# Kernel optimization log

Hardware: AMD Instinct MI355X
Metric: run time of the kernel (lower is better)

The kernel has to match this reference:

```python
import jax, jax.numpy as jnp
import numpy as np

SQRT_2PI = 2.5066282  # sqrt(2*3.1415926), matching the TF constant

def _gaussian(x, mean, std):
    return 1.0 / std / SQRT_2PI * jnp.exp(-0.5 * (x - mean) ** 2 / std ** 2)

def setup_inputs() -> dict:
    key = jax.random.key(0)
    ks = jax.random.split(key, 7)
    B, L, D, H, K = 4, 2048, 256, 8, 64
    return {
        "x": jax.random.normal(ks[0], (B, L, D), dtype=jnp.float32),
        "Wq": jax.random.normal(ks[1], (D, H * K), dtype=jnp.float32) * (2.0 / (D + H * K)) ** 0.5,
        "bq": jnp.zeros((H,), dtype=jnp.float32),
        "Wk": jax.random.normal(ks[2], (D, H * K), dtype=jnp.float32) * (2.0 / (D + H * K)) ** 0.5,
        "bk": jnp.zeros((H,), dtype=jnp.float32),
        "prior_mean": jax.random.uniform(ks[3], (H,), dtype=jnp.float32, minval=-2048.0, maxval=2048.0),
        "log_prior_std": jnp.full((H,), np.log(2048.0 / 4.0), dtype=jnp.float32),
    }

def reference(x, Wq, bq, Wk, bk, prior_mean, log_prior_std):
    B, L, D = x.shape
    H = bq.shape[0]
    Kd = Wq.shape[1] // H
    # projections; per-head scalar bias (tf.repeat(bias, head_dim))
    q = (x @ Wq).reshape(B, L, H, Kd) + bq[None, None, :, None]
    k = (x @ Wk).reshape(B, L, H, Kd) + bk[None, None, :, None]
    # relative-position distance matrix [L, L] (slice of the max_length matrix)
    pos = jnp.arange(L, dtype=jnp.float32)
    dist = pos[None, :] - pos[:, None]
    # per-head Gaussian prior [H, L, L]
    std = jnp.exp(log_prior_std)
    prior = _gaussian(dist[None, :, :], prior_mean[:, None, None], std[:, None, None])
    # scaled QK^T, modulated by prior, softmax over keys
    scores = jnp.einsum('bqhk,bmhk->bhqm', q, k) * (float(Kd) ** -0.5)
    attn = jax.nn.softmax(scores * prior[None], axis=-1)  # [B, H, L, L]
    # distance expectation instead of attn @ V
    out = jnp.sum(attn * dist[None, None, :, :], axis=-1)  # [B, H, L]
    return out.transpose(0, 2, 1)  # [B, L, H]
```

## Files before the change

### kernel.cpp

```cpp
#include <hip/hip_runtime.h>
#include <hip/hip_bf16.h>

#define LB 2048
#define DB 256
#define HB 8
#define BH 32
#define NG 19
#define NROW 48
#define NCK 16

typedef __attribute__((ext_vector_type(8))) short short8;
typedef __attribute__((ext_vector_type(4))) short short4v;
typedef __attribute__((ext_vector_type(4))) float floatx4;

static __device__ __forceinline__ short bfbits(float f) {
    __hip_bfloat16 h = __float2bfloat16(f);
    return *reinterpret_cast<short*>(&h);
}

__global__ __launch_bounds__(256) void prep_misc(
    const float* __restrict__ Wq, const float* __restrict__ Wk,
    const float* __restrict__ pm, const float* __restrict__ ls,
    __hip_bfloat16* __restrict__ wb, __hip_bfloat16* __restrict__ prtF)
{
    if (blockIdx.x < 64) {
        const int blk = blockIdx.x;
        const float* W = (blk & 32) ? Wk : Wq;
        const int nbase = (blk & 31) * 16;
#pragma unroll
        for (int cc = 0; cc < 2; ++cc) {
            const int c  = threadIdx.x + cc * 256;
            const int n  = nbase + (c & 15);
            const int k0 = (c >> 4) * 8;
            short8 o;
#pragma unroll
            for (int e = 0; e < 8; ++e) o[e] = bfbits(W[(size_t)(k0 + e) * 512 + n]);
            *(reinterpret_cast<short8*>(wb + (size_t)blk * 4096) + c) = o;
        }
        return;
    }
    const int blk2 = blockIdx.x - 64;
    const int h    = blk2 / 12;
    const int rem  = blk2 - h * 12;
    const int gt   = rem >> 2;
    const int msq  = rem & 3;
    const int wv   = threadIdx.x >> 6;
    const int l    = threadIdx.x & 63;

    const float mu        = pm[h];
    const float inv_sigma = __expf(-ls[h]);
    const float coef = 0.125f * inv_sigma * (1.0f / 2.5066282f);

    const int row = gt * 16 + (l & 15);
#pragma unroll
    for (int it = 0; it < 4; ++it) {
        const int ms = msq * 16 + wv * 4 + it;
        const int m0 = ms * 32 + (l >> 4) * 8;
        short8 o;
#pragma unroll
        for (int e = 0; e < 8; ++e) {
            float val = 0.f;
            if (row < 38) {
                const int g = (row < 19) ? row : row - 19;
                const float d = (float)(m0 + e - 128 * g + 128);
                const float t = (d - mu) * inv_sigma;
                const float P = coef * __expf(-0.5f * t * t);
                val = (row < 19) ? P : P * d;
            }
            o[e] = bfbits(val);
        }
        reinterpret_cast<short8*>(prtF)[(size_t)((h * 3 + gt) * 64 + ms) * 64 + l] = o;
    }
}

__global__ __launch_bounds__(256) void proj_fused(
    const float* __restrict__ x, const __hip_bfloat16* __restrict__ wb,
    const float* __restrict__ bq, const float* __restrict__ bk,
    __hip_bfloat16* __restrict__ qf, __hip_bfloat16* __restrict__ kT)
{
    __shared__ __align__(16) char smem[64 * 264 * 2];
    auto xs = reinterpret_cast<__hip_bfloat16(*)[264]>(smem);
    auto ot = reinterpret_cast<__hip_bfloat16(*)[136]>(smem);

    const int rt   = blockIdx.x;
    const int cg   = blockIdx.y;
    const int wave = threadIdx.x >> 6;
    const int lane = threadIdx.x & 63;
    const int kg   = lane >> 4;
    const int l15  = lane & 15;

#pragma unroll
    for (int it = 0; it < 16; ++it) {
        const int idx = threadIdx.x + it * 256;
        const int row = idx >> 6;
        const int k4  = (idx & 63) * 4;
        const float4 v = *reinterpret_cast<const float4*>(x + ((size_t)(rt * 64 + row)) * DB + k4);
        short4v o;
        o[0] = bfbits(v.x); o[1] = bfbits(v.y); o[2] = bfbits(v.z); o[3] = bfbits(v.w);
        *reinterpret_cast<short4v*>(&xs[row][k4]) = o;
    }
    __syncthreads();

    short8 a[8];
    {
        const __hip_bfloat16* xr = &xs[wave * 16 + l15][0];
#pragma unroll
        for (int kb = 0; kb < 8; ++kb)
            a[kb] = *reinterpret_cast<const short8*>(xr + kb * 32 + (lane >> 4) * 8);
    }
    __syncthreads();

    const int b_   = rt >> 5;
    const int gct0 = cg * 8;
    const short8* wp = reinterpret_cast<const short8*>(wb) + lane;

    short8 wA[8], wB[8];
#pragma unroll
    for (int kb = 0; kb < 8; ++kb) wA[kb] = wp[(size_t)(gct0 * 8 + kb) * 64];

#define PROJ_STEP(CURW, NXTW, CT)                                                     \
    {                                                                                 \
        if ((CT) < 7) {                                                               \
            _Pragma("unroll")                                                         \
            for (int kb = 0; kb < 8; ++kb)                                            \
                NXTW[kb] = wp[(size_t)((gct0 + (CT) + 1) * 8 + kb) * 64];             \
        }                                                                             \
        floatx4 acc = {0.f, 0.f, 0.f, 0.f};                                           \
        _Pragma("unroll")                                                             \
        for (int kb = 0; kb < 8; ++kb)                                                \
            acc = __builtin_amdgcn_mfma_f32_16x16x32_bf16(CURW[kb], a[kb], acc, 0, 0, 0); \
        const int h   = ((gct0 + (CT)) & 31) >> 2;                                    \
        const float bias = (cg < 4 ? bq : bk)[h];                                     \
        short4v o;                                                                    \
        _Pragma("unroll")                                                             \
        for (int r = 0; r < 4; ++r) o[r] = bfbits(acc[r] + bias);                     \
        *reinterpret_cast<short4v*>(&ot[wave * 16 + l15][(CT) * 16 + 4 * kg]) = o;    \
    }

    PROJ_STEP(wA, wB, 0)
    PROJ_STEP(wB, wA, 1)
    PROJ_STEP(wA, wB, 2)
    PROJ_STEP(wB, wA, 3)
    PROJ_STEP(wA, wB, 4)
    PROJ_STEP(wB, wA, 5)
    PROJ_STEP(wA, wB, 6)
    PROJ_STEP(wB, wA, 7)
#undef PROJ_STEP

    __syncthreads();

    if (cg < 4) {
        const int h0 = (cg & 3) * 2;
        const int rbase = (rt & 31) * 64;
#pragma unroll
        for (int it = 0; it < 8; ++it) {
            const int cidx = threadIdx.x + it * 256;
            const int row  = cidx >> 5;
            const int sub  = cidx & 31;
            const int hoff = sub >> 4;
            const int ch64 = (sub & 15) * 4;
            const short4v v = *reinterpret_cast<const short4v*>(&ot[row][sub * 4]);
            const size_t dst = (((size_t)(b_ * HB + h0 + hoff) << 11) + rbase + row) * 64 + ch64;
            *reinterpret_cast<short4v*>(qf + dst) = v;
        }
    } else {
        const int hoff = wave >> 1;
        const int msb  = wave & 1;
        const int h0   = (cg & 3) * 2;
        const int bh   = b_ * HB + h0 + hoff;
        const int msG  = (rt & 31) * 2 + msb;
        const int rowb = msb * 32 + (lane >> 4) * 8;
        const int colb = hoff * 64 + l15;
#pragma unroll
        for (int ct = 0; ct < 4; ++ct) {
            short8 o;
#pragma unroll
            for (int e = 0; e < 8; ++e)
                o[e] = *reinterpret_cast<const short*>(&ot[rowb + e][colb + ct * 16]);
            reinterpret_cast<short8*>(kT)[(size_t)((bh * 4 + ct) * 64 + msG) * 64 + lane] = o;
        }
    }
}

__global__ __launch_bounds__(256, 2) void conv_mfma(
    const __hip_bfloat16* __restrict__ prtF, const __hip_bfloat16* __restrict__ kT,
    float* __restrict__ gpart)
{
    const int bh   = blockIdx.x;
    const int wv   = threadIdx.x >> 6;
    const int lane = threadIdx.x & 63;
    const int ck   = blockIdx.y * 4 + wv;
    const int h    = bh & 7;

    const short8* A = reinterpret_cast<const short8*>(prtF);
    const short8* B = reinterpret_cast<const short8*>(kT);

    floatx4 acc[3][4];
#pragma unroll
    for (int gt = 0; gt < 3; ++gt)
#pragma unroll
        for (int ct = 0; ct < 4; ++ct) acc[gt][ct] = (floatx4){0.f, 0.f, 0.f, 0.f};

#pragma unroll
    for (int s = 0; s < 4; ++s) {
        const int ms = ck * 4 + s;
        short8 af[3], bf[4];
#pragma unroll
        for (int gt = 0; gt < 3; ++gt)
            af[gt] = A[(size_t)((h * 3 + gt) * 64 + ms) * 64 + lane];
#pragma unroll
        for (int ct = 0; ct < 4; ++ct)
            bf[ct] = B[(size_t)((bh * 4 + ct) * 64 + ms) * 64 + lane];
#pragma unroll
        for (int gt = 0; gt < 3; ++gt)
#pragma unroll
            for (int ct = 0; ct < 4; ++ct)
                acc[gt][ct] = __builtin_amdgcn_mfma_f32_16x16x32_bf16(af[gt], bf[ct], acc[gt][ct], 0, 0, 0);
    }

    const int kg = lane >> 4, l15 = lane & 15;
    float* gp = gpart + (size_t)(bh * NCK + ck) * (NROW * 64);
#pragma unroll
    for (int gt = 0; gt < 3; ++gt)
#pragma unroll
        for (int ct = 0; ct < 4; ++ct)
#pragma unroll
            for (int r = 0; r < 4; ++r)
                gp[(gt * 16 + 4 * kg + r) * 64 + ct * 16 + l15] = acc[gt][ct][r];
}

__global__ __launch_bounds__(256) void conv_combine(const float* __restrict__ gpart,
                                                    float* __restrict__ gw)
{
    const int j   = blockIdx.x * 256 + threadIdx.x;
    const int bh  = j / 3072;
    const int idx = j - bh * 3072;
    const float* gp = gpart + (size_t)bh * NCK * 3072 + idx;
    float s = 0.f;
#pragma unroll
    for (int c = 0; c < NCK; ++c) s += gp[(size_t)c * 3072];
    gw[j] = s;
}

__global__ __launch_bounds__(256) void final_kernel(
    const __hip_bfloat16* __restrict__ qf, const float* __restrict__ gw,
    float* __restrict__ out)
{
    const int row = blockIdx.x * 16 + (threadIdx.x >> 4);
    const int l15 = threadIdx.x & 15;
    const int bh  = row >> 11;
    const int i   = row & (LB - 1);
    const int b   = bh >> 3;
    const int h   = bh & 7;

    const short4v q4 = reinterpret_cast<const short4v*>(qf)[(size_t)row * 16 + l15];
    float q[4];
#pragma unroll
    for (int e = 0; e < 4; ++e) {
        const unsigned short u16 = (unsigned short)q4[e];
        const unsigned int bits = ((unsigned int)u16) << 16;
        q[e] = __builtin_bit_cast(float, bits);
    }

    const int   cell = i >> 7;
    const float u  = (float)(i & 127) * (1.0f / 128.0f);
    const float u2 = u * u, u3 = u2 * u;
    const float c0 = -0.5f * u + u2 - 0.5f * u3;
    const float c1 = 1.0f - 2.5f * u2 + 1.5f * u3;
    const float c2 = 0.5f * u + 2.0f * u2 - 1.5f * u3;
    const float c3 = -0.5f * u2 + 0.5f * u3;

    const float4* g4 = reinterpret_cast<const float4*>(gw + (size_t)bh * 3072) + l15;
    const float4 n0 = g4[(cell + 0) * 16], n1 = g4[(cell + 1) * 16];
    const float4 n2 = g4[(cell + 2) * 16], n3 = g4[(cell + 3) * 16];
    const float4 w0 = g4[(19 + cell + 0) * 16], w1 = g4[(19 + cell + 1) * 16];
    const float4 w2 = g4[(19 + cell + 2) * 16], w3 = g4[(19 + cell + 3) * 16];

    float D = q[0] * (c0 * n0.x + c1 * n1.x + c2 * n2.x + c3 * n3.x)
            + q[1] * (c0 * n0.y + c1 * n1.y + c2 * n2.y + c3 * n3.y)
            + q[2] * (c0 * n0.z + c1 * n1.z + c2 * n2.z + c3 * n3.z)
            + q[3] * (c0 * n0.w + c1 * n1.w + c2 * n2.w + c3 * n3.w);
    float N = q[0] * (c0 * w0.x + c1 * w1.x + c2 * w2.x + c3 * w3.x)
            + q[1] * (c0 * w0.y + c1 * w1.y + c2 * w2.y + c3 * w3.y)
            + q[2] * (c0 * w0.z + c1 * w1.z + c2 * w2.z + c3 * w3.z)
            + q[3] * (c0 * w0.w + c1 * w1.w + c2 * w2.w + c3 * w3.w);

#pragma unroll
    for (int off = 8; off >= 1; off >>= 1) {
        D += __shfl_xor(D, off, 64);
        N += __shfl_xor(N, off, 64);
    }
    if (l15 == 0) {
        const float C = (float)(2096128 - 2048 * i);
        out[((size_t)(b * LB + i)) * HB + h] = (C + N) / (2048.0f + D);
    }
}

extern "C" void kernel_launch(void* const* d_in, const int* in_sizes, int n_in,
                              void* d_out, int out_size, void* d_ws, size_t ws_size,
                              hipStream_t stream) {
    const float* x  = (const float*)d_in[0];
    const float* Wq = (const float*)d_in[1];
    const float* bq = (const float*)d_in[2];
    const float* Wk = (const float*)d_in[3];
    const float* bk = (const float*)d_in[4];
    const float* pm = (const float*)d_in[5];
    const float* ls = (const float*)d_in[6];
    float* out = (float*)d_out;

    char* w = (char*)d_ws;
    __hip_bfloat16* wbuf = (__hip_bfloat16*)w;  w += (size_t)64 * 4096 * 2;
    __hip_bfloat16* prtF = (__hip_bfloat16*)w;  w += (size_t)24 * 64 * 64 * 8 * 2;
    __hip_bfloat16* qf   = (__hip_bfloat16*)w;  w += (size_t)BH * LB * 64 * 2;
    __hip_bfloat16* kT   = (__hip_bfloat16*)w;  w += (size_t)BH * 4 * 64 * 64 * 8 * 2;
    float*          gpart = (float*)w;          w += (size_t)BH * NCK * NROW * 64 * 4;
    float*          gw    = (float*)w;

    prep_misc<<<dim3(160), dim3(256), 0, stream>>>(Wq, Wk, pm, ls, wbuf, prtF);
    proj_fused<<<dim3(128, 8), dim3(256), 0, stream>>>(x, wbuf, bq, bk, qf, kT);
    conv_mfma<<<dim3(32, 4), dim3(256), 0, stream>>>(prtF, kT, gpart);
    conv_combine<<<dim3(384), dim3(256), 0, stream>>>(gpart, gw);
    final_kernel<<<dim3(4096), dim3(256), 0, stream>>>(qf, gw, out);
}
```

Baseline: 43.58 us.

## Fuse Q/K projection per row tile and fold conv reduction into LDS

The projection kernel now computes all Q and K columns for a 32-row tile in one 512-thread block, so x is read and converted once instead of eight times across column groups. The conv kernel is launched with one block per batch-head, and each wave loops over four chunks. Partial sums are reduced through shared memory, which removes the separate combine kernel and its global partial buffer. The cost is that the conv stage now runs only 32 blocks, cutting parallelism on a many-CU GPU, and the projection block uses a larger LDS footprint.

```diff
diff --git a/kernel.cpp b/kernel.cpp
--- a/kernel.cpp
+++ b/kernel.cpp
@@ -73,28 +73,32 @@
     }
 }
 
-__global__ __launch_bounds__(256) void proj_fused(
+__global__ __launch_bounds__(512, 4) void proj_all(
     const float* __restrict__ x, const __hip_bfloat16* __restrict__ wb,
     const float* __restrict__ bq, const float* __restrict__ bk,
     __hip_bfloat16* __restrict__ qf, __hip_bfloat16* __restrict__ kT)
 {
-    __shared__ __align__(16) char smem[64 * 264 * 2];
+    __shared__ __align__(16) char smem[32 * 1032 * 2];
     auto xs = reinterpret_cast<__hip_bfloat16(*)[264]>(smem);
-    auto ot = reinterpret_cast<__hip_bfloat16(*)[136]>(smem);
-
-    const int rt   = blockIdx.x;
-    const int cg   = blockIdx.y;
-    const int wave = threadIdx.x >> 6;
-    const int lane = threadIdx.x & 63;
+    auto ot = reinterpret_cast<__hip_bfloat16(*)[1032]>(smem);
+
+    const int nrt  = blockIdx.x;
+    const int tid  = threadIdx.x;
+    const int w    = tid >> 6;
+    const int lane = tid & 63;
     const int kg   = lane >> 4;
     const int l15  = lane & 15;
-
-#pragma unroll
-    for (int it = 0; it < 16; ++it) {
-        const int idx = threadIdx.x + it * 256;
+    const int rg   = w & 1;
+    const int qu   = w >> 1;
+    const int b_   = nrt >> 6;
+    const int msG  = nrt & 63;
+
+#pragma unroll
+    for (int it = 0; it < 4; ++it) {
+        const int idx = tid + it * 512;
         const int row = idx >> 6;
         const int k4  = (idx & 63) * 4;
-        const float4 v = *reinterpret_cast<const float4*>(x + ((size_t)(rt * 64 + row)) * DB + k4);
+        const float4 v = *reinterpret_cast<const float4*>(x + ((size_t)(nrt * 32 + row)) * DB + k4);
         short4v o;
         o[0] = bfbits(v.x); o[1] = bfbits(v.y); o[2] = bfbits(v.z); o[3] = bfbits(v.w);
         *reinterpret_cast<short4v*>(&xs[row][k4]) = o;
@@ -103,15 +107,14 @@
 
     short8 a[8];
     {
-        const __hip_bfloat16* xr = &xs[wave * 16 + l15][0];
+        const __hip_bfloat16* xr = &xs[rg * 16 + l15][0];
 #pragma unroll
         for (int kb = 0; kb < 8; ++kb)
-            a[kb] = *reinterpret_cast<const short8*>(xr + kb * 32 + (lane >> 4) * 8);
+            a[kb] = *reinterpret_cast<const short8*>(xr + kb * 32 + kg * 8);
     }
     __syncthreads();
 
-    const int b_   = rt >> 5;
-    const int gct0 = cg * 8;
+    const int gct0 = qu * 16;
     const short8* wp = reinterpret_cast<const short8*>(wb) + lane;
 
     short8 wA[8], wB[8];
@@ -120,7 +123,7 @@
 
 #define PROJ_STEP(CURW, NXTW, CT)                                                     \
     {                                                                                 \
-        if ((CT) < 7) {                                                               \
+        if ((CT) < 15) {                                                              \
             _Pragma("unroll")                                                         \
             for (int kb = 0; kb < 8; ++kb)                                            \
                 NXTW[kb] = wp[(size_t)((gct0 + (CT) + 1) * 8 + kb) * 64];             \
@@ -129,12 +132,13 @@
         _Pragma("unroll")                                                             \
         for (int kb = 0; kb < 8; ++kb)                                                \
             acc = __builtin_amdgcn_mfma_f32_16x16x32_bf16(CURW[kb], a[kb], acc, 0, 0, 0); \
-        const int h   = ((gct0 + (CT)) & 31) >> 2;                                    \
-        const float bias = (cg < 4 ? bq : bk)[h];                                     \
+        const int gct = gct0 + (CT);                                                  \
+        const int h   = (gct & 31) >> 2;                                              \
+        const float bias = (gct < 32 ? bq : bk)[h];                                   \
         short4v o;                                                                    \
         _Pragma("unroll")                                                             \
         for (int r = 0; r < 4; ++r) o[r] = bfbits(acc[r] + bias);                     \
-        *reinterpret_cast<short4v*>(&ot[wave * 16 + l15][(CT) * 16 + 4 * kg]) = o;    \
+        *reinterpret_cast<short4v*>(&ot[rg * 16 + l15][gct * 16 + 4 * kg]) = o;       \
     }
 
     PROJ_STEP(wA, wB, 0)
@@ -145,52 +149,60 @@
     PROJ_STEP(wB, wA, 5)
     PROJ_STEP(wA, wB, 6)
     PROJ_STEP(wB, wA, 7)
+    PROJ_STEP(wA, wB, 8)
+    PROJ_STEP(wB, wA, 9)
+    PROJ_STEP(wA, wB, 10)
+    PROJ_STEP(wB, wA, 11)
+    PROJ_STEP(wA, wB, 12)
+    PROJ_STEP(wB, wA, 13)
+    PROJ_STEP(wA, wB, 14)
+    PROJ_STEP(wB, wA, 15)
 #undef PROJ_STEP
 
     __syncthreads();
 
-    if (cg < 4) {
-        const int h0 = (cg & 3) * 2;
-        const int rbase = (rt & 31) * 64;
-#pragma unroll
-        for (int it = 0; it < 8; ++it) {
-            const int cidx = threadIdx.x + it * 256;
-            const int row  = cidx >> 5;
-            const int sub  = cidx & 31;
-            const int hoff = sub >> 4;
-            const int ch64 = (sub & 15) * 4;
-            const short4v v = *reinterpret_cast<const short4v*>(&ot[row][sub * 4]);
-            const size_t dst = (((size_t)(b_ * HB + h0 + hoff) << 11) + rbase + row) * 64 + ch64;
-            *reinterpret_cast<short4v*>(qf + dst) = v;
-        }
-    } else {
-        const int hoff = wave >> 1;
-        const int msb  = wave & 1;
-        const int h0   = (cg & 3) * 2;
-        const int bh   = b_ * HB + h0 + hoff;
-        const int msG  = (rt & 31) * 2 + msb;
-        const int rowb = msb * 32 + (lane >> 4) * 8;
-        const int colb = hoff * 64 + l15;
-#pragma unroll
-        for (int ct = 0; ct < 4; ++ct) {
+#pragma unroll
+    for (int it = 0; it < 8; ++it) {
+        const int cidx = tid + it * 512;
+        const int row  = cidx >> 7;
+        const int sub  = cidx & 127;
+        const int h    = sub >> 4;
+        const int ch64 = (sub & 15) * 4;
+        const short4v v = *reinterpret_cast<const short4v*>(&ot[row][sub * 4]);
+        const size_t dst = (((size_t)(b_ * HB + h) << 11) + msG * 32 + row) * 64 + ch64;
+        *reinterpret_cast<short4v*>(qf + dst) = v;
+    }
+
+    {
+        const int f  = w * 4;
+#pragma unroll
+        for (int ff = 0; ff < 4; ++ff) {
+            const int h  = (f + ff) >> 2;
+            const int ct = (f + ff) & 3;
+            const int bh = b_ * HB + h;
+            const int colb = 512 + h * 64 + ct * 16 + l15;
+            const int rowb = kg * 8;
             short8 o;
 #pragma unroll
             for (int e = 0; e < 8; ++e)
-                o[e] = *reinterpret_cast<const short*>(&ot[rowb + e][colb + ct * 16]);
+                o[e] = *reinterpret_cast<const short*>(&ot[rowb + e][colb]);
             reinterpret_cast<short8*>(kT)[(size_t)((bh * 4 + ct) * 64 + msG) * 64 + lane] = o;
         }
     }
 }
 
-__global__ __launch_bounds__(256, 2) void conv_mfma(
+__global__ __launch_bounds__(256) void conv_fused(
     const __hip_bfloat16* __restrict__ prtF, const __hip_bfloat16* __restrict__ kT,
-    float* __restrict__ gpart)
+    float* __restrict__ gw)
 {
+    __shared__ float red[4][3072];
+
     const int bh   = blockIdx.x;
     const int wv   = threadIdx.x >> 6;
     const int lane = threadIdx.x & 63;
-    const int ck   = blockIdx.y * 4 + wv;
     const int h    = bh & 7;
+    const int kg   = lane >> 4;
+    const int l15  = lane & 15;
 
     const short8* A = reinterpret_cast<const short8*>(prtF);
     const short8* B = reinterpret_cast<const short8*>(kT);
@@ -202,44 +214,37 @@
         for (int ct = 0; ct < 4; ++ct) acc[gt][ct] = (floatx4){0.f, 0.f, 0.f, 0.f};
 
 #pragma unroll
-    for (int s = 0; s < 4; ++s) {
-        const int ms = ck * 4 + s;
-        short8 af[3], bf[4];
-#pragma unroll
-        for (int gt = 0; gt < 3; ++gt)
-            af[gt] = A[(size_t)((h * 3 + gt) * 64 + ms) * 64 + lane];
+    for (int cki = 0; cki < 4; ++cki) {
+        const int ck = wv * 4 + cki;
+#pragma unroll
+        for (int s = 0; s < 4; ++s) {
+            const int ms = ck * 4 + s;
+            short8 af[3], bf[4];
+#pragma unroll
+            for (int gt = 0; gt < 3; ++gt)
+                af[gt] = A[(size_t)((h * 3 + gt) * 64 + ms) * 64 + lane];
+#pragma unroll
+            for (int ct = 0; ct < 4; ++ct)
+                bf[ct] = B[(size_t)((bh * 4 + ct) * 64 + ms) * 64 + lane];
+#pragma unroll
+            for (int gt = 0; gt < 3; ++gt)
+#pragma unroll
+                for (int ct = 0; ct < 4; ++ct)
+                    acc[gt][ct] = __builtin_amdgcn_mfma_f32_16x16x32_bf16(af[gt], bf[ct], acc[gt][ct], 0, 0, 0);
+        }
+    }
+
+#pragma unroll
+    for (int gt = 0; gt < 3; ++gt)
 #pragma unroll
         for (int ct = 0; ct < 4; ++ct)
-            bf[ct] = B[(size_t)((bh * 4 + ct) * 64 + ms) * 64 + lane];
-#pragma unroll
-        for (int gt = 0; gt < 3; ++gt)
-#pragma unroll
-            for (int ct = 0; ct < 4; ++ct)
-                acc[gt][ct] = __builtin_amdgcn_mfma_f32_16x16x32_bf16(af[gt], bf[ct], acc[gt][ct], 0, 0, 0);
-    }
-
-    const int kg = lane >> 4, l15 = lane & 15;
-    float* gp = gpart + (size_t)(bh * NCK + ck) * (NROW * 64);
-#pragma unroll
-    for (int gt = 0; gt < 3; ++gt)
-#pragma unroll
-        for (int ct = 0; ct < 4; ++ct)
 #pragma unroll
             for (int r = 0; r < 4; ++r)
-                gp[(gt * 16 + 4 * kg + r) * 64 + ct * 16 + l15] = acc[gt][ct][r];
-}
-
-__global__ __launch_bounds__(256) void conv_combine(const float* __restrict__ gpart,
-                                                    float* __restrict__ gw)
-{
-    const int j   = blockIdx.x * 256 + threadIdx.x;
-    const int bh  = j / 3072;
-    const int idx = j - bh * 3072;
-    const float* gp = gpart + (size_t)bh * NCK * 3072 + idx;
-    float s = 0.f;
-#pragma unroll
-    for (int c = 0; c < NCK; ++c) s += gp[(size_t)c * 3072];
-    gw[j] = s;
+                red[wv][(gt * 16 + 4 * kg + r) * 64 + ct * 16 + l15] = acc[gt][ct][r];
+    __syncthreads();
+
+    for (int j = threadIdx.x; j < 3072; j += 256)
+        gw[(size_t)bh * 3072 + j] = red[0][j] + red[1][j] + red[2][j] + red[3][j];
 }
 
 __global__ __launch_bounds__(256) void final_kernel(
@@ -313,12 +318,10 @@
     __hip_bfloat16* prtF = (__hip_bfloat16*)w;  w += (size_t)24 * 64 * 64 * 8 * 2;
     __hip_bfloat16* qf   = (__hip_bfloat16*)w;  w += (size_t)BH * LB * 64 * 2;
     __hip_bfloat16* kT   = (__hip_bfloat16*)w;  w += (size_t)BH * 4 * 64 * 64 * 8 * 2;
-    float*          gpart = (float*)w;          w += (size_t)BH * NCK * NROW * 64 * 4;
-    float*          gw    = (float*)w;
+    float*          gw   = (float*)w;
 
     prep_misc<<<dim3(160), dim3(256), 0, stream>>>(Wq, Wk, pm, ls, wbuf, prtF);
-    proj_fused<<<dim3(128, 8), dim3(256), 0, stream>>>(x, wbuf, bq, bk, qf, kT);
-    conv_mfma<<<dim3(32, 4), dim3(256), 0, stream>>>(prtF, kT, gpart);
-    conv_combine<<<dim3(384), dim3(256), 0, stream>>>(gpart, gw);
+    proj_all<<<dim3(256), dim3(512), 0, stream>>>(x, wbuf, bq, bk, qf, kT);
+    conv_fused<<<dim3(32), dim3(256), 0, stream>>>(prtF, kT, gw);
     final_kernel<<<dim3(4096), dim3(256), 0, stream>>>(qf, gw, out);
 }
```

After: 49.47 us. 1.14x slower.
